# Optimization experiments

Measured on AMD Instinct MI355X. Metric: run time of the kernel, lower is better.

Reference implementation:

```python
import jax, jax.numpy as jnp
import numpy as np

B, S, D, H = 4, 2048, 1024, 16
HD = D // H


def setup_inputs() -> dict:
    key = jax.random.key(0)
    k1, k2, k3 = jax.random.split(key, 3)
    x = jax.random.normal(k1, (B, S, D), dtype=jnp.float32)
    w_qkv = jax.random.normal(k2, (D, 3 * D), dtype=jnp.float32) * (1.0 / np.sqrt(D))
    w_out = jax.random.normal(k3, (D, D), dtype=jnp.float32) * (1.0 / np.sqrt(D))
    return {"x": x, "w_qkv": w_qkv, "w_out": w_out}


def reference(x, w_qkv, w_out):
    bsz, seq_len, d = x.shape
    qkv = x @ w_qkv  # [B, S, 3D]
    q, k, v = jnp.split(qkv, 3, axis=-1)
    # [B, H, S, HD]
    q = q.reshape(bsz, seq_len, H, HD).transpose(0, 2, 1, 3)
    k = k.reshape(bsz, seq_len, H, HD).transpose(0, 2, 1, 3)
    v = v.reshape(bsz, seq_len, H, HD).transpose(0, 2, 1, 3)
    scale = 1.0 / np.sqrt(HD)
    scores = jnp.einsum('bhqd,bhkd->bhqk', q, k) * scale  # [B, H, S, S]
    causal = jnp.tril(jnp.ones((seq_len, seq_len), dtype=bool))
    scores = jnp.where(causal[None, None], scores, -jnp.inf)
    weights = jax.nn.softmax(scores, axis=-1)
    ctx = jnp.einsum('bhqk,bhkd->bhqd', weights, v)
    ctx = ctx.transpose(0, 2, 1, 3).reshape(bsz, seq_len, d)
    return ctx @ w_out
```

## Files before the change

kernel.cpp:

```cpp
#include <hip/hip_runtime.h>
#include <stdint.h>

typedef unsigned short u16;
typedef __attribute__((ext_vector_type(4))) float f32x4;
typedef __attribute__((ext_vector_type(8))) __bf16 bf16x8;
typedef __attribute__((ext_vector_type(8))) u16 u16x8;
typedef __attribute__((ext_vector_type(4))) u16 u16x4;
typedef __attribute__((ext_vector_type(2))) unsigned u32x2;

static constexpr int kB = 4, kS = 2048, kD = 1024, kH = 16, kHD = 64;
static constexpr int M1 = kB * kS;
static constexpr int N1 = 3 * kD;
static constexpr int K1 = kD;

#define SCLF 0.18033688011112042f
#define MFMA16(a, b, c) __builtin_amdgcn_mfma_f32_16x16x32_bf16((a), (b), (c), 0, 0, 0)

union U4 { unsigned u[4]; bf16x8 v; };

__device__ __forceinline__ u16 f2bf(float f) {
  union { float f; uint32_t u; } c; c.f = f;
  uint32_t u = c.u + 0x7FFFu + ((c.u >> 16) & 1u);
  return (u16)(u >> 16);
}

__device__ __forceinline__ unsigned pkbf(float a, float b) {
  union { __bf16 h[2]; unsigned u; } c;
  c.h[0] = (__bf16)a; c.h[1] = (__bf16)b;
  return c.u;
}

__device__ __forceinline__ void gload_lds16(const u16* g, u16* l) {
  __builtin_amdgcn_global_load_lds(
      (const __attribute__((address_space(1))) unsigned int*)g,
      (__attribute__((address_space(3))) unsigned int*)l, 16, 0, 0);
}

__global__ __launch_bounds__(256) void k_cast_x(const float* __restrict__ x,
                                                u16* __restrict__ o) {
  int i = (blockIdx.x * 256 + threadIdx.x) * 4;
  f32x4 v = *(const f32x4*)(x + i);
  u16x4 r;
  r[0] = f2bf(v[0]); r[1] = f2bf(v[1]); r[2] = f2bf(v[2]); r[3] = f2bf(v[3]);
  *(u16x4*)(o + i) = r;
}

__global__ __launch_bounds__(256) void k_transpose_cast(const float* __restrict__ w,
                                                        u16* __restrict__ wt,
                                                        int K, int N) {
  __shared__ float t[32][33];
  const int n0 = blockIdx.x * 32, k0 = blockIdx.y * 32;
  const int tx = threadIdx.x & 31, ty = threadIdx.x >> 5;
  for (int r = ty; r < 32; r += 8)
    t[r][tx] = w[(size_t)(k0 + r) * N + n0 + tx];
  __syncthreads();
  for (int r = ty; r < 32; r += 8)
    wt[(size_t)(n0 + r) * K + k0 + tx] = f2bf(t[tx][r]);
}

template <int MODE>
__global__ __launch_bounds__(512) void k_gemm_bt(const u16* __restrict__ A,
                                                 const u16* __restrict__ BT,
                                                 u16* __restrict__ obf,
                                                 float* __restrict__ of,
                                                 int M, int N, int K) {
  __shared__ __align__(16) u16 Asb[3][128 * 64];
  __shared__ __align__(16) u16 Bsb[3][256 * 64];

  const int tid = threadIdx.x;
  const int wave = tid >> 6, lane = tid & 63;
  const int l15 = lane & 15, l16 = lane >> 4;

  const int bid = blockIdx.x;
  const int qch = gridDim.x >> 3;
  const int swz = (bid & 7) * qch + (bid >> 3);
  const int ntN = N >> 8;
  const int row0 = (swz / ntN) * 128, col0 = (swz % ntN) * 256;
  const int wm = (wave >> 2) * 64, wn = (wave & 3) * 64;

  f32x4 acc[4][4];
#pragma unroll
  for (int i = 0; i < 4; ++i)
#pragma unroll
    for (int j = 0; j < 4; ++j) acc[i][j] = f32x4{0.f, 0.f, 0.f, 0.f};

  const int lr = lane >> 3, ls = lane & 7;
  const u16* srcA[2];
#pragma unroll
  for (int j = 0; j < 2; ++j) {
    const int r = (wave * 2 + j) * 8 + lr;
    srcA[j] = A + (size_t)(row0 + r) * K + (ls ^ (r & 7)) * 8;
  }
  const u16* srcB[4];
#pragma unroll
  for (int j = 0; j < 4; ++j) {
    const int r = (wave * 4 + j) * 8 + lr;
    srcB[j] = BT + (size_t)(col0 + r) * K + (ls ^ (r & 7)) * 8;
  }

  const int nT = K >> 6;

#define STAGE(t)                                                        \
  {                                                                     \
    const int buf_ = (t) % 3;                                           \
    const int kt_ = (t) * 64;                                           \
    _Pragma("unroll")                                                   \
    for (int j = 0; j < 2; ++j)                                         \
      gload_lds16(srcA[j] + kt_, &Asb[buf_][(wave * 2 + j) * 512]);     \
    _Pragma("unroll")                                                   \
    for (int j = 0; j < 4; ++j)                                         \
      gload_lds16(srcB[j] + kt_, &Bsb[buf_][(wave * 4 + j) * 512]);     \
  }

  STAGE(0);
  STAGE(1);

  for (int t = 0; t < nT; ++t) {
    if (t + 1 < nT) asm volatile("s_waitcnt vmcnt(6)" ::: "memory");
    else            asm volatile("s_waitcnt vmcnt(0)" ::: "memory");
    __builtin_amdgcn_s_barrier();
    __builtin_amdgcn_sched_barrier(0);

    if (t + 2 < nT) STAGE(t + 2);

    const u16* As = &Asb[t % 3][0];
    const u16* Bs = &Bsb[t % 3][0];
#pragma unroll
    for (int kk = 0; kk < 2; ++kk) {
      bf16x8 af[4], bfv[4];
#pragma unroll
      for (int f = 0; f < 4; ++f) {
        const int ra = wm + f * 16 + l15;
        af[f] = *(const bf16x8*)&As[ra * 64 + (((kk * 4 + l16) ^ (ra & 7)) * 8)];
        const int rb = wn + f * 16 + l15;
        bfv[f] = *(const bf16x8*)&Bs[rb * 64 + (((kk * 4 + l16) ^ (rb & 7)) * 8)];
      }
      __builtin_amdgcn_s_setprio(1);
#pragma unroll
      for (int fm = 0; fm < 4; ++fm)
#pragma unroll
        for (int fn = 0; fn < 4; ++fn)
          acc[fm][fn] = MFMA16(af[fm], bfv[fn], acc[fm][fn]);
      __builtin_amdgcn_s_setprio(0);
    }
  }

#pragma unroll
  for (int fm = 0; fm < 4; ++fm)
#pragma unroll
    for (int fn = 0; fn < 4; ++fn) {
      const int n = col0 + wn + fn * 16 + l15;
#pragma unroll
      for (int j = 0; j < 4; ++j) {
        const int m = row0 + wm + fm * 16 + l16 * 4 + j;
        float v = acc[fm][fn][j];
        if constexpr (MODE == 0) {
          const int which = n >> 10, d = n & 1023;
          const int h = d >> 6, hd = d & 63;
          const int b = m >> 11, s = m & 2047;
          if (which == 0) v *= SCLF;
          obf[((((size_t)which * 4 + b) * 16 + h) * 2048 + s) * 64 + hd] = f2bf(v);
        } else {
          of[(size_t)m * N + n] = v;
        }
      }
    }
#undef STAGE
}

__global__ __launch_bounds__(512, 4) void k_attn(const u16* __restrict__ Qg,
                                                 const u16* __restrict__ Kg,
                                                 const u16* __restrict__ Vg,
                                                 u16* __restrict__ ctx) {
  __shared__ __align__(16) u16 Ks[2][64 * 64];
  __shared__ __align__(16) unsigned Vt[2][2048];
  __shared__ __align__(16) unsigned Pl[8 * 256];

  const int bid = blockIdx.x;
  const int xcd = bid & 7, i2 = bid >> 3;
  const int bh = xcd * 8 + (i2 & 7);
  const int p = i2 >> 3;
  const int bb = bh >> 4, hh = bh & 15;
  const int tid = threadIdx.x;
  const int wave = tid >> 6, lane = tid & 63;
  const int l15 = lane & 15, l16 = lane >> 4;

  const u16* Qb = Qg + (size_t)bh * kS * kHD;
  const u16* Kb = Kg + (size_t)bh * kS * kHD;
  const u16* Vb = Vg + (size_t)bh * kS * kHD;

  const int kkey = tid >> 3, ksl = tid & 7;
  const int do4 = tid & 15, kp = tid >> 4;
  unsigned* Pw = Pl + wave * 256 + l15 * 16;
  const int pm = ((l15 >> 1) & 3) << 2;

  unsigned voff[4];
#pragma unroll
  for (int i = 0; i < 4; ++i) {
    const int d = do4 * 4 + i;
    voff[i] = d * 32 + (kp ^ ((((d & 7) ^ (d >> 3))) << 2));
  }
  const u16* ksrc = Kb + (size_t)kkey * 64 + (ksl ^ (kkey & 7)) * 8;

  for (int phase = 0; phase < 2; ++phase) {
    const int qsup = phase ? (15 - p) : p;
    const int qstart = qsup * 128 + wave * 16;
    const int ntiles = 2 * qsup + 2;

    bf16x8 bq[2];
#pragma unroll
    for (int ds = 0; ds < 2; ++ds)
      bq[ds] = *(const bf16x8*)(Qb + (size_t)(qstart + l15) * 64 + ds * 32 + l16 * 8);

    f32x4 acc[4];
#pragma unroll
    for (int i = 0; i < 4; ++i) acc[i] = f32x4{0.f, 0.f, 0.f, 0.f};
    float mrow = -3e38f, lrowh = 0.f;

    __syncthreads();

    u16x4 va, vb;
    {
      const u16* vs = Vb + (size_t)(2 * kp) * 64 + do4 * 4;
      va = *(const u16x4*)vs; vb = *(const u16x4*)(vs + 64);
    }
#pragma unroll
    for (int i = 0; i < 4; ++i)
      Vt[0][voff[i]] = (unsigned)va[i] | ((unsigned)vb[i] << 16);
    {
      const u16* vs = Vb + (size_t)(64 + 2 * kp) * 64 + do4 * 4;
      va = *(const u16x4*)vs; vb = *(const u16x4*)(vs + 64);
    }
    gload_lds16(ksrc, &Ks[0][wave * 512]);

    for (int t = 0; t < ntiles; ++t) {
      const int kv0 = t * 64;
      __syncthreads();

      if (t + 1 < ntiles) {
        const int nb = (t + 1) & 1;
#pragma unroll
        for (int i = 0; i < 4; ++i)
          Vt[nb][voff[i]] = (unsigned)va[i] | ((unsigned)vb[i] << 16);
        gload_lds16(ksrc + (size_t)(t + 1) * 64 * 64, &Ks[nb][wave * 512]);
        if (t + 2 < ntiles) {
          const u16* vs = Vb + (size_t)((t + 2) * 64 + 2 * kp) * 64 + do4 * 4;
          va = *(const u16x4*)vs; vb = *(const u16x4*)(vs + 64);
        }
      }

      if (kv0 > qstart + 15) continue;

      const u16* Ksb = &Ks[t & 1][0];
      const unsigned* Vtb = &Vt[t & 1][0];
      const int qv = qstart + l15;

#pragma unroll
      for (int c = 0; c < 2; ++c) {
        const int kb = kv0 + 32 * c;
        if (kb > qstart + 15) continue;

        f32x4 st0 = f32x4{0.f, 0.f, 0.f, 0.f}, st1 = st0;
        __builtin_amdgcn_s_setprio(1);
#pragma unroll
        for (int ds = 0; ds < 2; ++ds) {
          const int slot = ((ds * 4 + l16) ^ (l15 & 7)) * 8;
          bf16x8 ak0 = *(const bf16x8*)&Ksb[(c * 32 + l15) * 64 + slot];
          st0 = MFMA16(ak0, bq[ds], st0);
          bf16x8 ak1 = *(const bf16x8*)&Ksb[(c * 32 + 16 + l15) * 64 + slot];
          st1 = MFMA16(ak1, bq[ds], st1);
        }
        __builtin_amdgcn_s_setprio(0);

        float tl;
        if (kb + 31 > qstart) {
#pragma unroll
          for (int j = 0; j < 4; ++j) {
            const int key = kb + l16 * 4 + j;
            st0[j] = (key <= qv) ? st0[j] : -3e38f;
            st1[j] = (key + 16 <= qv) ? st1[j] : -3e38f;
          }
        }
        tl = fmaxf(fmaxf(fmaxf(st0[0], st0[1]), fmaxf(st0[2], st0[3])),
                   fmaxf(fmaxf(st1[0], st1[1]), fmaxf(st1[2], st1[3])));

        float mn;
        if (__all(tl <= mrow + 8.0f)) {
          mn = mrow;
        } else {
          float tj = fmaxf(tl, __shfl_xor(tl, 16, 64));
          tj = fmaxf(tj, __shfl_xor(tj, 32, 64));
          mn = fmaxf(mrow, tj);
          const float al = exp2f(mrow - mn);
          mrow = mn;
          lrowh *= al;
#pragma unroll
          for (int i = 0; i < 4; ++i)
#pragma unroll
            for (int j = 0; j < 4; ++j) acc[i][j] *= al;
        }

#pragma unroll
        for (int j = 0; j < 4; ++j) {
          st0[j] = exp2f(st0[j] - mn);
          st1[j] = exp2f(st1[j] - mn);
        }
        lrowh += ((st0[0] + st0[1]) + (st0[2] + st0[3])) +
                 ((st1[0] + st1[1]) + (st1[2] + st1[3]));

        {
          const unsigned p0 = pkbf(st0[0], st0[1]);
          const unsigned p1 = pkbf(st0[2], st0[3]);
          const unsigned p2 = pkbf(st1[0], st1[1]);
          const unsigned p3 = pkbf(st1[2], st1[3]);
          *(u32x2*)&Pw[(l16 * 2) ^ pm] = u32x2{p0, p1};
          *(u32x2*)&Pw[(8 + l16 * 2) ^ pm] = u32x2{p2, p3};
        }
        U4 f;
        f = *(const U4*)&Pw[(l16 * 4) ^ pm];

        __builtin_amdgcn_s_setprio(1);
#pragma unroll
        for (int dg = 0; dg < 4; ++dg) {
          const int d = dg * 16 + l15;
          const int addr = d * 32 + ((c * 16 + l16 * 4) ^ ((((d & 7) ^ (d >> 3))) << 2));
          const bf16x8 vf = *(const bf16x8*)&Vtb[addr];
          acc[dg] = MFMA16(vf, f.v, acc[dg]);
        }
        __builtin_amdgcn_s_setprio(0);
      }
    }

    float l2 = lrowh + __shfl_xor(lrowh, 16, 64);
    const float lrow = l2 + __shfl_xor(l2, 32, 64);
    const float rl = 1.0f / lrow;
    u16* orow = ctx + ((size_t)bb * kS + (qstart + l15)) * kD + hh * 64;
#pragma unroll
    for (int dg = 0; dg < 4; ++dg) {
      u16x4 pk;
#pragma unroll
      for (int j = 0; j < 4; ++j) pk[j] = f2bf(acc[dg][j] * rl);
      *(u16x4*)&orow[dg * 16 + l16 * 4] = pk;
    }
  }
}

extern "C" void kernel_launch(void* const* d_in, const int* in_sizes, int n_in,
                              void* d_out, int out_size, void* d_ws, size_t ws_size,
                              hipStream_t stream) {
  const float* x     = (const float*)d_in[0];
  const float* w_qkv = (const float*)d_in[1];
  const float* w_out = (const float*)d_in[2];
  float* out = (float*)d_out;

  u16* ws    = (u16*)d_ws;
  u16* x_bf  = ws;
  u16* wqkvT = x_bf + (size_t)M1 * K1;
  u16* woutT = wqkvT + (size_t)N1 * K1;
  u16* qkv   = woutT + (size_t)kD * kD;
  u16* ctx   = qkv + (size_t)3 * kB * kH * kS * kHD;

  k_cast_x<<<M1 * K1 / 1024, 256, 0, stream>>>(x, x_bf);
  k_transpose_cast<<<dim3(N1 / 32, K1 / 32), 256, 0, stream>>>(w_qkv, wqkvT, K1, N1);
  k_transpose_cast<<<dim3(kD / 32, kD / 32), 256, 0, stream>>>(w_out, woutT, kD, kD);

  k_gemm_bt<0><<<dim3(768), 512, 0, stream>>>(x_bf, wqkvT, qkv, nullptr,
                                              M1, N1, K1);

  const u16* Qg = qkv;
  const u16* Kg = qkv + (size_t)kB * kH * kS * kHD;
  const u16* Vg = qkv + (size_t)2 * kB * kH * kS * kHD;
  k_attn<<<dim3(512), 512, 0, stream>>>(Qg, Kg, Vg, ctx);

  k_gemm_bt<1><<<dim3(256), 512, 0, stream>>>(ctx, woutT, nullptr, out,
                                              M1, kD, K1);
}
```

Before: 202.4 us.

## Double attention KV tile to 128 keys and process 64-key softmax chunks

The attention kernel now stages 128 keys of K and transposed V per pipeline step instead of 64, which halves the number of tiles and block-wide barriers per query block. Each inner step handles 64 keys at once, so the online-softmax max/rescale check runs once per 64 keys rather than per 32. The cost is double the LDS footprint (about 72KB per block versus 40KB), which may lower occupancy against the launch bound of 4 blocks. It also adds more registers for the score tiles and V prefetch, and wastes more masked work on the diagonal tile.

```diff
diff --git a/kernel.cpp b/kernel.cpp
--- a/kernel.cpp
+++ b/kernel.cpp
@@ -172,8 +172,8 @@
                                                  const u16* __restrict__ Kg,
                                                  const u16* __restrict__ Vg,
                                                  u16* __restrict__ ctx) {
-  __shared__ __align__(16) u16 Ks[2][64 * 64];
-  __shared__ __align__(16) unsigned Vt[2][2048];
+  __shared__ __align__(16) u16 Ks[2][128 * 64];
+  __shared__ __align__(16) unsigned Vt[2][4096];
   __shared__ __align__(16) unsigned Pl[8 * 256];
 
   const int bid = blockIdx.x;
@@ -198,14 +198,14 @@
 #pragma unroll
   for (int i = 0; i < 4; ++i) {
     const int d = do4 * 4 + i;
-    voff[i] = d * 32 + (kp ^ ((((d & 7) ^ (d >> 3))) << 2));
+    voff[i] = d * 64 + (kp ^ ((((d & 7) ^ (d >> 3))) << 2));
   }
   const u16* ksrc = Kb + (size_t)kkey * 64 + (ksl ^ (kkey & 7)) * 8;
 
   for (int phase = 0; phase < 2; ++phase) {
     const int qsup = phase ? (15 - p) : p;
     const int qstart = qsup * 128 + wave * 16;
-    const int ntiles = 2 * qsup + 2;
+    const int ntiles = qsup + 1;
 
     bf16x8 bq[2];
 #pragma unroll
@@ -219,33 +219,44 @@
 
     __syncthreads();
 
-    u16x4 va, vb;
-    {
-      const u16* vs = Vb + (size_t)(2 * kp) * 64 + do4 * 4;
-      va = *(const u16x4*)vs; vb = *(const u16x4*)(vs + 64);
-    }
-#pragma unroll
-    for (int i = 0; i < 4; ++i)
-      Vt[0][voff[i]] = (unsigned)va[i] | ((unsigned)vb[i] << 16);
-    {
-      const u16* vs = Vb + (size_t)(64 + 2 * kp) * 64 + do4 * 4;
-      va = *(const u16x4*)vs; vb = *(const u16x4*)(vs + 64);
+    u16x4 va[2], vb[2];
+#pragma unroll
+    for (int r = 0; r < 2; ++r) {
+      const u16* vs = Vb + (size_t)(2 * (kp + 32 * r)) * 64 + do4 * 4;
+      va[r] = *(const u16x4*)vs; vb[r] = *(const u16x4*)(vs + 64);
+    }
+#pragma unroll
+    for (int r = 0; r < 2; ++r)
+#pragma unroll
+      for (int i = 0; i < 4; ++i)
+        Vt[0][voff[i] + 32 * r] = (unsigned)va[r][i] | ((unsigned)vb[r][i] << 16);
+#pragma unroll
+    for (int r = 0; r < 2; ++r) {
+      const u16* vs = Vb + (size_t)(128 + 2 * (kp + 32 * r)) * 64 + do4 * 4;
+      va[r] = *(const u16x4*)vs; vb[r] = *(const u16x4*)(vs + 64);
     }
     gload_lds16(ksrc, &Ks[0][wave * 512]);
+    gload_lds16(ksrc + 4096, &Ks[0][4096 + wave * 512]);
 
     for (int t = 0; t < ntiles; ++t) {
-      const int kv0 = t * 64;
+      const int kv0 = t * 128;
       __syncthreads();
 
       if (t + 1 < ntiles) {
         const int nb = (t + 1) & 1;
 #pragma unroll
-        for (int i = 0; i < 4; ++i)
-          Vt[nb][voff[i]] = (unsigned)va[i] | ((unsigned)vb[i] << 16);
-        gload_lds16(ksrc + (size_t)(t + 1) * 64 * 64, &Ks[nb][wave * 512]);
+        for (int r = 0; r < 2; ++r)
+#pragma unroll
+          for (int i = 0; i < 4; ++i)
+            Vt[nb][voff[i] + 32 * r] = (unsigned)va[r][i] | ((unsigned)vb[r][i] << 16);
+        gload_lds16(ksrc + (size_t)(t + 1) * 8192, &Ks[nb][wave * 512]);
+        gload_lds16(ksrc + (size_t)(t + 1) * 8192 + 4096, &Ks[nb][4096 + wave * 512]);
         if (t + 2 < ntiles) {
-          const u16* vs = Vb + (size_t)((t + 2) * 64 + 2 * kp) * 64 + do4 * 4;
-          va = *(const u16x4*)vs; vb = *(const u16x4*)(vs + 64);
+#pragma unroll
+          for (int r = 0; r < 2; ++r) {
+            const u16* vs = Vb + (size_t)((t + 2) * 128 + 2 * (kp + 32 * r)) * 64 + do4 * 4;
+            va[r] = *(const u16x4*)vs; vb[r] = *(const u16x4*)(vs + 64);
+          }
         }
       }
 
@@ -256,33 +267,38 @@
       const int qv = qstart + l15;
 
 #pragma unroll
-      for (int c = 0; c < 2; ++c) {
-        const int kb = kv0 + 32 * c;
+      for (int h = 0; h < 2; ++h) {
+        const int kb = kv0 + 64 * h;
         if (kb > qstart + 15) continue;
 
-        f32x4 st0 = f32x4{0.f, 0.f, 0.f, 0.f}, st1 = st0;
+        f32x4 st[4];
+#pragma unroll
+        for (int g = 0; g < 4; ++g) st[g] = f32x4{0.f, 0.f, 0.f, 0.f};
         __builtin_amdgcn_s_setprio(1);
 #pragma unroll
         for (int ds = 0; ds < 2; ++ds) {
           const int slot = ((ds * 4 + l16) ^ (l15 & 7)) * 8;
-          bf16x8 ak0 = *(const bf16x8*)&Ksb[(c * 32 + l15) * 64 + slot];
-          st0 = MFMA16(ak0, bq[ds], st0);
-          bf16x8 ak1 = *(const bf16x8*)&Ksb[(c * 32 + 16 + l15) * 64 + slot];
-          st1 = MFMA16(ak1, bq[ds], st1);
+#pragma unroll
+          for (int g = 0; g < 4; ++g) {
+            bf16x8 ak = *(const bf16x8*)&Ksb[(64 * h + 16 * g + l15) * 64 + slot];
+            st[g] = MFMA16(ak, bq[ds], st[g]);
+          }
         }
         __builtin_amdgcn_s_setprio(0);
 
-        float tl;
-        if (kb + 31 > qstart) {
-#pragma unroll
-          for (int j = 0; j < 4; ++j) {
-            const int key = kb + l16 * 4 + j;
-            st0[j] = (key <= qv) ? st0[j] : -3e38f;
-            st1[j] = (key + 16 <= qv) ? st1[j] : -3e38f;
-          }
-        }
-        tl = fmaxf(fmaxf(fmaxf(st0[0], st0[1]), fmaxf(st0[2], st0[3])),
-                   fmaxf(fmaxf(st1[0], st1[1]), fmaxf(st1[2], st1[3])));
+        if (kb + 63 > qstart) {
+#pragma unroll
+          for (int g = 0; g < 4; ++g)
+#pragma unroll
+            for (int j = 0; j < 4; ++j) {
+              const int key = kb + 16 * g + l16 * 4 + j;
+              st[g][j] = (key <= qv) ? st[g][j] : -3e38f;
+            }
+        }
+        float tl = -3e38f;
+#pragma unroll
+        for (int g = 0; g < 4; ++g)
+          tl = fmaxf(tl, fmaxf(fmaxf(st[g][0], st[g][1]), fmaxf(st[g][2], st[g][3])));
 
         float mn;
         if (__all(tl <= mrow + 8.0f)) {
@@ -301,33 +317,35 @@
         }
 
 #pragma unroll
-        for (int j = 0; j < 4; ++j) {
-          st0[j] = exp2f(st0[j] - mn);
-          st1[j] = exp2f(st1[j] - mn);
-        }
-        lrowh += ((st0[0] + st0[1]) + (st0[2] + st0[3])) +
-                 ((st1[0] + st1[1]) + (st1[2] + st1[3]));
-
-        {
-          const unsigned p0 = pkbf(st0[0], st0[1]);
-          const unsigned p1 = pkbf(st0[2], st0[3]);
-          const unsigned p2 = pkbf(st1[0], st1[1]);
-          const unsigned p3 = pkbf(st1[2], st1[3]);
+        for (int g = 0; g < 4; ++g)
+#pragma unroll
+          for (int j = 0; j < 4; ++j) st[g][j] = exp2f(st[g][j] - mn);
+#pragma unroll
+        for (int g = 0; g < 4; ++g)
+          lrowh += (st[g][0] + st[g][1]) + (st[g][2] + st[g][3]);
+
+#pragma unroll
+        for (int s2 = 0; s2 < 2; ++s2) {
+          const unsigned p0 = pkbf(st[2 * s2][0], st[2 * s2][1]);
+          const unsigned p1 = pkbf(st[2 * s2][2], st[2 * s2][3]);
+          const unsigned p2 = pkbf(st[2 * s2 + 1][0], st[2 * s2 + 1][1]);
+          const unsigned p3 = pkbf(st[2 * s2 + 1][2], st[2 * s2 + 1][3]);
           *(u32x2*)&Pw[(l16 * 2) ^ pm] = u32x2{p0, p1};
           *(u32x2*)&Pw[(8 + l16 * 2) ^ pm] = u32x2{p2, p3};
-        }
-        U4 f;
-        f = *(const U4*)&Pw[(l16 * 4) ^ pm];
-
-        __builtin_amdgcn_s_setprio(1);
-#pragma unroll
-        for (int dg = 0; dg < 4; ++dg) {
-          const int d = dg * 16 + l15;
-          const int addr = d * 32 + ((c * 16 + l16 * 4) ^ ((((d & 7) ^ (d >> 3))) << 2));
-          const bf16x8 vf = *(const bf16x8*)&Vtb[addr];
-          acc[dg] = MFMA16(vf, f.v, acc[dg]);
-        }
-        __builtin_amdgcn_s_setprio(0);
+          U4 f;
+          f = *(const U4*)&Pw[(l16 * 4) ^ pm];
+
+          const int ckp = 32 * h + 16 * s2;
+          __builtin_amdgcn_s_setprio(1);
+#pragma unroll
+          for (int dg = 0; dg < 4; ++dg) {
+            const int d = dg * 16 + l15;
+            const int addr = d * 64 + ((ckp + l16 * 4) ^ ((((d & 7) ^ (d >> 3))) << 2));
+            const bf16x8 vf = *(const bf16x8*)&Vtb[addr];
+            acc[dg] = MFMA16(vf, f.v, acc[dg]);
+          }
+          __builtin_amdgcn_s_setprio(0);
+        }
       }
     }
 
```

Result: slower. 207.9 us (+2.7%).
